# Optimization experiments

Hardware: AMD Instinct MI355X
Metric: run time of the kernel (lower is better)

Reference implementation:

```python
import jax, jax.numpy as jnp
import numpy as np

QMIN, QMAX = -128.0, 127.0  # 8-bit signed activation range


def fq_act(x, s):
    """Fake-quantize activations: clip(round(x/s))*s with straight-through estimator."""
    y = jnp.clip(jnp.round(x / s), QMIN, QMAX) * s
    return x + jax.lax.stop_gradient(y - x)


def fq_weight(w):
    """Per-tensor max-abs symmetric (narrow-range) 8-bit weight fake-quant with STE."""
    s = jnp.max(jnp.abs(w)) / 127.0
    y = jnp.clip(jnp.round(w / s), -127.0, 127.0) * s
    return w + jax.lax.stop_gradient(y - w)


def conv1x1(x, w, b):
    # x: [b,c,h,w], w: [o,c] -> [b,o,h,w]
    return jnp.einsum('bchw,oc->bohw', x, w) + b[None, :, None, None]


def setup_inputs() -> dict:
    key = jax.random.key(0)
    ks = jax.random.split(key, 6)
    B, C, HC, H, W = 8, 64, 32, 64, 64
    x = jax.random.normal(ks[0], (B, C, H, W), dtype=jnp.float32)
    wq = jax.random.normal(ks[1], (HC, C), dtype=jnp.float32) * 0.05
    wk = jax.random.normal(ks[2], (HC, C), dtype=jnp.float32) * 0.05
    wv = jax.random.normal(ks[3], (HC, C), dtype=jnp.float32) * 0.05
    wp = jax.random.normal(ks[4], (C, HC), dtype=jnp.float32) * 0.05
    return {
        'x': x,
        'wq': wq, 'bq': jnp.zeros((HC,), jnp.float32),
        'wk': wk, 'bk': jnp.zeros((HC,), jnp.float32),
        'wv': wv, 'bv': jnp.zeros((HC,), jnp.float32),
        'wp': wp, 'bp': jnp.zeros((C,), jnp.float32),
        's_in': jnp.ones((1,), jnp.float32) * 0.0625,
        's_out': jnp.ones((1,), jnp.float32) * 0.0625,
    }


def reference(x, wq, bq, wk, bk, wv, bv, wp, bp, s_in, s_out):
    b, c, h, w = x.shape
    hc = wq.shape[0]
    n = h * w
    xq = fq_act(x, s_in)                              # quant_inp(x)
    q = conv1x1(xq, fq_weight(wq), bq).reshape(b, hc, n).transpose(0, 2, 1)  # [b,n,hc]
    k = conv1x1(xq, fq_weight(wk), bk).reshape(b, hc, n)                     # [b,hc,n]
    v = conv1x1(xq, fq_weight(wv), bv).reshape(b, hc, n).transpose(0, 2, 1)  # [b,n,hc]
    z = jax.nn.softmax(jnp.einsum('bqc,bck->bqk', q, k), axis=-1)            # [b,n,n]
    z = jnp.einsum('bqk,bkc->bqc', z, v).transpose(0, 2, 1).reshape(b, hc, h, w)
    z = fq_act(z, s_in)                               # quant_inp(z) (shared module/scale)
    out = xq + conv1x1(z, fq_weight(wp), bp)
    return fq_act(out, s_out)                         # self.act QuantIdentity
```

## Files before the change

kernel.cpp:

```cpp
#include <hip/hip_runtime.h>
#include <hip/hip_bf16.h>
#include <cstdint>
#include <cstddef>

#define NB 8
#define NC 64
#define NHC 32
#define NN 4096
#define LOG2E 1.44269504088896340736f

typedef short v8s __attribute__((ext_vector_type(8)));
typedef float v4f __attribute__((ext_vector_type(4)));
typedef unsigned int v4u __attribute__((ext_vector_type(4)));

__device__ __forceinline__ unsigned short f2b(float f) {
    unsigned int u = __builtin_bit_cast(unsigned int, f);
    u += 0x7fffu + ((u >> 16) & 1u);
    return (unsigned short)(u >> 16);
}
__device__ __forceinline__ float b2f(unsigned short s) {
    unsigned int u = ((unsigned int)s) << 16;
    return __builtin_bit_cast(float, u);
}
__device__ __forceinline__ unsigned int pack2_bf16(float a, float b) {
    unsigned int ua = __builtin_bit_cast(unsigned int, a);
    ua += 0x7fffu + ((ua >> 16) & 1u);
    unsigned int ub = __builtin_bit_cast(unsigned int, b);
    ub += 0x7fffu + ((ub >> 16) & 1u);
    return (ua >> 16) | (ub & 0xffff0000u);
}
__device__ __forceinline__ unsigned int trunc2_bf16(float a, float b) {
    return __builtin_amdgcn_perm(__builtin_bit_cast(unsigned int, b),
                                 __builtin_bit_cast(unsigned int, a), 0x07060302u);
}
__device__ __forceinline__ float wave_max(float v) {
    #pragma unroll
    for (int off = 1; off < 64; off <<= 1) v = fmaxf(v, __shfl_xor(v, off));
    return v;
}

__global__ __launch_bounds__(256) void k_qkv(
    const float* __restrict__ x,
    const float* __restrict__ wq, const float* __restrict__ wk, const float* __restrict__ wv,
    const float* __restrict__ bq, const float* __restrict__ bk, const float* __restrict__ bv,
    const float* __restrict__ s_in,
    unsigned short* __restrict__ xqb, unsigned short* __restrict__ qb,
    unsigned short* __restrict__ kb, unsigned short* __restrict__ vb)
{
    int blk = blockIdx.x;
    int b   = blk >> 6;
    int p0  = (blk & 63) * 64;
    int tid = threadIdx.x;
    int wave = tid >> 6;
    int lane = tid & 63;

    __shared__ __align__(16) unsigned short xt[64][72];
    __shared__ __align__(16) unsigned short wlds[6144];
    __shared__ float red[3][4];

    float4 q0 = *(const float4*)(wq + tid * 8), q1 = *(const float4*)(wq + tid * 8 + 4);
    float4 k0 = *(const float4*)(wk + tid * 8), k1 = *(const float4*)(wk + tid * 8 + 4);
    float4 v0 = *(const float4*)(wv + tid * 8), v1 = *(const float4*)(wv + tid * 8 + 4);
    float mq = fmaxf(fmaxf(fmaxf(fabsf(q0.x), fabsf(q0.y)), fmaxf(fabsf(q0.z), fabsf(q0.w))),
                     fmaxf(fmaxf(fabsf(q1.x), fabsf(q1.y)), fmaxf(fabsf(q1.z), fabsf(q1.w))));
    float mk = fmaxf(fmaxf(fmaxf(fabsf(k0.x), fabsf(k0.y)), fmaxf(fabsf(k0.z), fabsf(k0.w))),
                     fmaxf(fmaxf(fabsf(k1.x), fabsf(k1.y)), fmaxf(fabsf(k1.z), fabsf(k1.w))));
    float mv = fmaxf(fmaxf(fmaxf(fabsf(v0.x), fabsf(v0.y)), fmaxf(fabsf(v0.z), fabsf(v0.w))),
                     fmaxf(fmaxf(fabsf(v1.x), fabsf(v1.y)), fmaxf(fabsf(v1.z), fabsf(v1.w))));
    mq = wave_max(mq); mk = wave_max(mk); mv = wave_max(mv);
    if (lane == 0) { red[0][wave] = mq; red[1][wave] = mk; red[2][wave] = mv; }
    __syncthreads();
    float sq = fmaxf(fmaxf(red[0][0], red[0][1]), fmaxf(red[0][2], red[0][3])) / 127.0f;
    float sk = fmaxf(fmaxf(red[1][0], red[1][1]), fmaxf(red[1][2], red[1][3])) / 127.0f;
    float sw = fmaxf(fmaxf(red[2][0], red[2][1]), fmaxf(red[2][2], red[2][3])) / 127.0f;
    {
        float eq[8] = {q0.x, q0.y, q0.z, q0.w, q1.x, q1.y, q1.z, q1.w};
        float ek[8] = {k0.x, k0.y, k0.z, k0.w, k1.x, k1.y, k1.z, k1.w};
        float ev[8] = {v0.x, v0.y, v0.z, v0.w, v1.x, v1.y, v1.z, v1.w};
        #pragma unroll
        for (int j = 0; j < 8; ++j) {
            wlds[0 * 2048 + tid * 8 + j] = f2b(fminf(fmaxf(rintf(eq[j] / sq), -127.f), 127.f) * sq);
            wlds[1 * 2048 + tid * 8 + j] = f2b(fminf(fmaxf(rintf(ek[j] / sk), -127.f), 127.f) * sk);
            wlds[2 * 2048 + tid * 8 + j] = f2b(fminf(fmaxf(rintf(ev[j] / sw), -127.f), 127.f) * sw);
        }
    }

    float sv = s_in[0];
    float sinv = 1.0f / sv;
    int jj = tid & 15;
    int c0 = tid >> 4;
    #pragma unroll
    for (int it = 0; it < 4; ++it) {
        int c = c0 + it * 16;
        size_t gi = ((size_t)(b * NC + c) << 12) + p0 + jj * 4;
        float4 xv = *(const float4*)(x + gi);
        float r0 = fminf(fmaxf(rintf(xv.x * sinv), -128.f), 127.f) * sv;
        float r1 = fminf(fmaxf(rintf(xv.y * sinv), -128.f), 127.f) * sv;
        float r2 = fminf(fmaxf(rintf(xv.z * sinv), -128.f), 127.f) * sv;
        float r3 = fminf(fmaxf(rintf(xv.w * sinv), -128.f), 127.f) * sv;
        *(uint2*)(xqb + gi) = make_uint2(pack2_bf16(r0, r1), pack2_bf16(r2, r3));
        xt[jj * 4 + 0][c] = f2b(r0);
        xt[jj * 4 + 1][c] = f2b(r1);
        xt[jj * 4 + 2][c] = f2b(r2);
        xt[jj * 4 + 3][c] = f2b(r3);
    }
    __syncthreads();

    int quad = lane >> 4;
    int l15  = lane & 15;

    v8s bf0 = *(const v8s*)(&xt[wave * 16 + l15][0  + quad * 8]);
    v8s bf1 = *(const v8s*)(&xt[wave * 16 + l15][32 + quad * 8]);

    int pos = p0 + wave * 16 + l15;
    size_t posg = (size_t)b * NN + pos;
    int posP = p0 + (wave >> 1) * 32 + (l15 >> 2) * 8 + (wave & 1) * 4 + (l15 & 3);
    const v4f zc = {0.f, 0.f, 0.f, 0.f};

    #pragma unroll
    for (int rb = 0; rb < 6; ++rb) {
        v8s a0 = *(const v8s*)(wlds + (rb * 16 + l15) * 64 + 0  + quad * 8);
        v8s a1 = *(const v8s*)(wlds + (rb * 16 + l15) * 64 + 32 + quad * 8);
        v4f t   = __builtin_amdgcn_mfma_f32_16x16x32_bf16(a0, bf0, zc, 0, 0, 0);
        v4f acc = __builtin_amdgcn_mfma_f32_16x16x32_bf16(a1, bf1, t, 0, 0, 0);

        int R0 = rb * 16 + quad * 4;
        float vals[4];
        #pragma unroll
        for (int r = 0; r < 4; ++r) {
            int R = R0 + r;
            float bias = (R < 32) ? bq[R] : (R < 64) ? bk[R - 32] : bv[R - 64];
            float vv = acc[r] + bias;
            if (R < 32) vv *= LOG2E;
            vals[r] = vv;
        }
        if (R0 < 32) {
            *(unsigned int*)(qb + posg * NHC + R0)     = pack2_bf16(vals[0], vals[1]);
            *(unsigned int*)(qb + posg * NHC + R0 + 2) = pack2_bf16(vals[2], vals[3]);
        } else if (R0 < 64) {
            *(unsigned int*)(kb + posg * NHC + R0 - 32)     = pack2_bf16(vals[0], vals[1]);
            *(unsigned int*)(kb + posg * NHC + R0 - 32 + 2) = pack2_bf16(vals[2], vals[3]);
        } else {
            #pragma unroll
            for (int r = 0; r < 4; ++r)
                vb[(size_t)(b * NHC + R0 - 64 + r) * NN + posP] = f2b(vals[r]);
        }
    }
}

__global__ __launch_bounds__(256, 2) void k_attn(
    const unsigned short* __restrict__ qb, const unsigned short* __restrict__ kb,
    const unsigned short* __restrict__ vb, const unsigned short* __restrict__ xqb,
    const float* __restrict__ wp, const float* __restrict__ bp,
    const float* __restrict__ s_in, const float* __restrict__ s_out,
    float* __restrict__ out)
{
    int blk  = blockIdx.x;
    int b    = blk >> 6;
    int qt   = blk & 63;
    int qbase = qt * 64;
    int tid  = threadIdx.x;
    int wave = tid >> 6;
    int lane = tid & 63;
    int quad = lane >> 4;
    int l15  = lane & 15;

    __shared__ __align__(16) float zbuf[4][64][36];
    __shared__ float lbuf[4][64];
    __shared__ __align__(16) unsigned short wpq[2048];
    __shared__ float redw[4];

    {
        float4 a0 = *(const float4*)(wp + tid * 8), a1 = *(const float4*)(wp + tid * 8 + 4);
        float mx = fmaxf(fmaxf(fmaxf(fabsf(a0.x), fabsf(a0.y)), fmaxf(fabsf(a0.z), fabsf(a0.w))),
                         fmaxf(fmaxf(fabsf(a1.x), fabsf(a1.y)), fmaxf(fabsf(a1.z), fabsf(a1.w))));
        mx = wave_max(mx);
        if (lane == 0) redw[wave] = mx;
        __syncthreads();
        float scale = fmaxf(fmaxf(redw[0], redw[1]), fmaxf(redw[2], redw[3])) / 127.0f;
        float e[8] = {a0.x, a0.y, a0.z, a0.w, a1.x, a1.y, a1.z, a1.w};
        #pragma unroll
        for (int j = 0; j < 8; ++j) {
            float r = fminf(fmaxf(rintf(e[j] / scale), -127.f), 127.f);
            wpq[tid * 8 + j] = f2b(r * scale);
        }
    }

    const unsigned short* qbat = qb + (size_t)b * NN * NHC;
    const unsigned short* kbat = kb + (size_t)b * NN * NHC;
    const unsigned short* vbat = vb + (size_t)b * NHC * NN;

    v8s qf[4];
    #pragma unroll
    for (int s = 0; s < 4; ++s)
        qf[s] = *(const v8s*)(qbat + (qbase + s * 16 + l15) * NHC + quad * 8);

    const v4f zc = {0.f, 0.f, 0.f, 0.f};
    v4f zt[4][2] = {{zc, zc}, {zc, zc}, {zc, zc}, {zc, zc}};
    float psA[4] = {0.f, 0.f, 0.f, 0.f};
    float psB[4] = {0.f, 0.f, 0.f, 0.f};

    int k0 = wave * 1024;
    const unsigned short* vrow0 = vbat + (size_t)( 0 + l15) * NN;
    const unsigned short* vrow1 = vbat + (size_t)(16 + l15) * NN;

    v8s ck0 = *(const v8s*)(kbat + (k0 +  0 + l15) * NHC + quad * 8);
    v8s ck1 = *(const v8s*)(kbat + (k0 + 16 + l15) * NHC + quad * 8);
    v8s ck2 = *(const v8s*)(kbat + (k0 + 32 + l15) * NHC + quad * 8);
    v8s ck3 = *(const v8s*)(kbat + (k0 + 48 + l15) * NHC + quad * 8);
    v8s cv00 = *(const v8s*)(vrow0 + k0      + quad * 8);
    v8s cv01 = *(const v8s*)(vrow0 + k0 + 32 + quad * 8);
    v8s cv10 = *(const v8s*)(vrow1 + k0      + quad * 8);
    v8s cv11 = *(const v8s*)(vrow1 + k0 + 32 + quad * 8);

    #pragma unroll 1
    for (int i = 0; i < 16; ++i) {
        int nki = k0 + (((i + 1) & 15) << 6);
        v8s nk0 = *(const v8s*)(kbat + (nki +  0 + l15) * NHC + quad * 8);
        v8s nk1 = *(const v8s*)(kbat + (nki + 16 + l15) * NHC + quad * 8);
        v8s nk2 = *(const v8s*)(kbat + (nki + 32 + l15) * NHC + quad * 8);
        v8s nk3 = *(const v8s*)(kbat + (nki + 48 + l15) * NHC + quad * 8);
        v8s nv00 = *(const v8s*)(vrow0 + nki      + quad * 8);
        v8s nv01 = *(const v8s*)(vrow0 + nki + 32 + quad * 8);
        v8s nv10 = *(const v8s*)(vrow1 + nki      + quad * 8);
        v8s nv11 = *(const v8s*)(vrow1 + nki + 32 + quad * 8);

        #pragma unroll
        for (int s = 0; s < 4; ++s) {
            v4f sa[4];
            __builtin_amdgcn_s_setprio(1);
            sa[0] = __builtin_amdgcn_mfma_f32_16x16x32_bf16(ck0, qf[s], zc, 0, 0, 0);
            sa[1] = __builtin_amdgcn_mfma_f32_16x16x32_bf16(ck1, qf[s], zc, 0, 0, 0);
            sa[2] = __builtin_amdgcn_mfma_f32_16x16x32_bf16(ck2, qf[s], zc, 0, 0, 0);
            sa[3] = __builtin_amdgcn_mfma_f32_16x16x32_bf16(ck3, qf[s], zc, 0, 0, 0);
            __builtin_amdgcn_s_setprio(0);

            #pragma unroll
            for (int g = 0; g < 2; ++g) {
                float p00 = __builtin_amdgcn_exp2f(sa[2 * g][0]);
                float p01 = __builtin_amdgcn_exp2f(sa[2 * g][1]);
                float p02 = __builtin_amdgcn_exp2f(sa[2 * g][2]);
                float p03 = __builtin_amdgcn_exp2f(sa[2 * g][3]);
                float p10 = __builtin_amdgcn_exp2f(sa[2 * g + 1][0]);
                float p11 = __builtin_amdgcn_exp2f(sa[2 * g + 1][1]);
                float p12 = __builtin_amdgcn_exp2f(sa[2 * g + 1][2]);
                float p13 = __builtin_amdgcn_exp2f(sa[2 * g + 1][3]);
                psA[s] += p00 + p01;
                psB[s] += p02 + p03;
                psA[s] += p10 + p11;
                psB[s] += p12 + p13;
                v4u w;
                w.x = trunc2_bf16(p00, p01);
                w.y = trunc2_bf16(p02, p03);
                w.z = trunc2_bf16(p10, p11);
                w.w = trunc2_bf16(p12, p13);
                v8s pfrag = __builtin_bit_cast(v8s, w);
                __builtin_amdgcn_s_setprio(1);
                if (g == 0) {
                    zt[s][0] = __builtin_amdgcn_mfma_f32_16x16x32_bf16(cv00, pfrag, zt[s][0], 0, 0, 0);
                    zt[s][1] = __builtin_amdgcn_mfma_f32_16x16x32_bf16(cv10, pfrag, zt[s][1], 0, 0, 0);
                } else {
                    zt[s][0] = __builtin_amdgcn_mfma_f32_16x16x32_bf16(cv01, pfrag, zt[s][0], 0, 0, 0);
                    zt[s][1] = __builtin_amdgcn_mfma_f32_16x16x32_bf16(cv11, pfrag, zt[s][1], 0, 0, 0);
                }
                __builtin_amdgcn_s_setprio(0);
            }
        }
        ck0 = nk0; ck1 = nk1; ck2 = nk2; ck3 = nk3;
        cv00 = nv00; cv01 = nv01; cv10 = nv10; cv11 = nv11;
    }

    #pragma unroll
    for (int s = 0; s < 4; ++s) {
        *(v4f*)(&zbuf[wave][s * 16 + l15][     quad * 4]) = zt[s][0];
        *(v4f*)(&zbuf[wave][s * 16 + l15][16 + quad * 4]) = zt[s][1];
        float ps = psA[s] + psB[s];
        ps += __shfl_xor(ps, 16);
        ps += __shfl_xor(ps, 32);
        if (quad == 0) lbuf[wave][s * 16 + l15] = ps;
    }
    __syncthreads();

    int myq = wave * 16 + l15;
    float L = lbuf[0][myq] + lbuf[1][myq] + lbuf[2][myq] + lbuf[3][myq];

    float z[8] = {0.f};
    #pragma unroll
    for (int w = 0; w < 4; ++w) {
        v4f za  = *(const v4f*)(&zbuf[w][myq][quad * 8]);
        v4f zb2 = *(const v4f*)(&zbuf[w][myq][quad * 8 + 4]);
        #pragma unroll
        for (int j = 0; j < 4; ++j) { z[j] += za[j]; z[4 + j] += zb2[j]; }
    }
    float sv = s_in[0], sinv = 1.0f / sv;
    float so = s_out[0], soinv = 1.0f / so;
    float Linv = 1.0f / L;
    unsigned int zp[4];
    #pragma unroll
    for (int jp = 0; jp < 4; ++jp) {
        float a = z[2 * jp]     * Linv;
        float c = z[2 * jp + 1] * Linv;
        a = fminf(fmaxf(rintf(a * sinv), -128.f), 127.f) * sv;
        c = fminf(fmaxf(rintf(c * sinv), -128.f), 127.f) * sv;
        zp[jp] = pack2_bf16(a, c);
    }
    v8s zf = __builtin_bit_cast(v8s, *(uint4*)zp);

    v8s w0f = *(const v8s*)(wpq + ( 0 + l15) * NHC + quad * 8);
    v8s w1f = *(const v8s*)(wpq + (16 + l15) * NHC + quad * 8);
    v8s w2f = *(const v8s*)(wpq + (32 + l15) * NHC + quad * 8);
    v8s w3f = *(const v8s*)(wpq + (48 + l15) * NHC + quad * 8);
    v4f o0 = __builtin_amdgcn_mfma_f32_16x16x32_bf16(w0f, zf, zc, 0, 0, 0);
    v4f o1 = __builtin_amdgcn_mfma_f32_16x16x32_bf16(w1f, zf, zc, 0, 0, 0);
    v4f o2 = __builtin_amdgcn_mfma_f32_16x16x32_bf16(w2f, zf, zc, 0, 0, 0);
    v4f o3 = __builtin_amdgcn_mfma_f32_16x16x32_bf16(w3f, zf, zc, 0, 0, 0);

    int pos = qbase + wave * 16 + l15;
    #pragma unroll
    for (int ot = 0; ot < 4; ++ot) {
        v4f ov = (ot == 0) ? o0 : (ot == 1) ? o1 : (ot == 2) ? o2 : o3;
        #pragma unroll
        for (int r = 0; r < 4; ++r) {
            int oc = ot * 16 + quad * 4 + r;
            size_t idx = (size_t)(b * NC + oc) * NN + pos;
            float val = ov[r] + bp[oc] + b2f(xqb[idx]);
            float f = fminf(fmaxf(rintf(val * soinv), -128.f), 127.f);
            out[idx] = f * so;
        }
    }
}

extern "C" void kernel_launch(void* const* d_in, const int* in_sizes, int n_in,
                              void* d_out, int out_size, void* d_ws, size_t ws_size,
                              hipStream_t stream) {
    const float* x     = (const float*)d_in[0];
    const float* wq    = (const float*)d_in[1];
    const float* bq    = (const float*)d_in[2];
    const float* wk    = (const float*)d_in[3];
    const float* bk    = (const float*)d_in[4];
    const float* wv    = (const float*)d_in[5];
    const float* bv    = (const float*)d_in[6];
    const float* wp    = (const float*)d_in[7];
    const float* bp    = (const float*)d_in[8];
    const float* s_in  = (const float*)d_in[9];
    const float* s_out = (const float*)d_in[10];
    float* out = (float*)d_out;

    char* ws = (char*)d_ws;
    size_t off = 0;
    auto carve = [&](size_t bytes) {
        void* p = ws + off;
        off = (off + bytes + 255) & ~(size_t)255;
        return p;
    };
    unsigned short* xqb = (unsigned short*)carve((size_t)NB * NC * NN * 2);
    unsigned short* qbf = (unsigned short*)carve((size_t)NB * NN * NHC * 2);
    unsigned short* kbf = (unsigned short*)carve((size_t)NB * NN * NHC * 2);
    unsigned short* vbf = (unsigned short*)carve((size_t)NB * NHC * NN * 2);

    hipLaunchKernelGGL(k_qkv, dim3(512), dim3(256), 0, stream,
                       x, wq, wk, wv, bq, bk, bv, s_in, xqb, qbf, kbf, vbf);
    hipLaunchKernelGGL(k_attn, dim3(512), dim3(256), 0, stream,
                       qbf, kbf, vbf, xqb, wp, bp, s_in, s_out, out);
}
```

Measured before the change: 112.4 us.

## Halve QKV projection tile to 32 positions and interleave batch in block index

```diff
diff --git a/kernel.cpp b/kernel.cpp
--- a/kernel.cpp
+++ b/kernel.cpp
@@ -39,7 +39,7 @@
     return v;
 }
 
-__global__ __launch_bounds__(256) void k_qkv(
+__global__ __launch_bounds__(256, 4) void k_qkv(
     const float* __restrict__ x,
     const float* __restrict__ wq, const float* __restrict__ wk, const float* __restrict__ wv,
     const float* __restrict__ bq, const float* __restrict__ bk, const float* __restrict__ bv,
@@ -48,19 +48,26 @@
     unsigned short* __restrict__ kb, unsigned short* __restrict__ vb)
 {
     int blk = blockIdx.x;
-    int b   = blk >> 6;
-    int p0  = (blk & 63) * 64;
+    int b   = blk & 7;
+    int p0  = (blk >> 3) * 32;
     int tid = threadIdx.x;
     int wave = tid >> 6;
     int lane = tid & 63;
 
-    __shared__ __align__(16) unsigned short xt[64][72];
+    __shared__ __align__(16) unsigned short xt[32][72];
     __shared__ __align__(16) unsigned short wlds[6144];
     __shared__ float red[3][4];
 
     float4 q0 = *(const float4*)(wq + tid * 8), q1 = *(const float4*)(wq + tid * 8 + 4);
     float4 k0 = *(const float4*)(wk + tid * 8), k1 = *(const float4*)(wk + tid * 8 + 4);
     float4 v0 = *(const float4*)(wv + tid * 8), v1 = *(const float4*)(wv + tid * 8 + 4);
+    int jj = tid & 7;
+    int c0 = tid >> 3;
+    size_t gi0 = ((size_t)(b * NC + c0) << 12) + p0 + jj * 4;
+    size_t gi1 = ((size_t)(b * NC + c0 + 32) << 12) + p0 + jj * 4;
+    float4 xv0 = *(const float4*)(x + gi0);
+    float4 xv1 = *(const float4*)(x + gi1);
+
     float mq = fmaxf(fmaxf(fmaxf(fabsf(q0.x), fabsf(q0.y)), fmaxf(fabsf(q0.z), fabsf(q0.w))),
                      fmaxf(fmaxf(fabsf(q1.x), fabsf(q1.y)), fmaxf(fabsf(q1.z), fabsf(q1.w))));
     float mk = fmaxf(fmaxf(fmaxf(fabsf(k0.x), fabsf(k0.y)), fmaxf(fabsf(k0.z), fabsf(k0.w))),
@@ -87,38 +94,46 @@
 
     float sv = s_in[0];
     float sinv = 1.0f / sv;
-    int jj = tid & 15;
-    int c0 = tid >> 4;
-    #pragma unroll
-    for (int it = 0; it < 4; ++it) {
-        int c = c0 + it * 16;
-        size_t gi = ((size_t)(b * NC + c) << 12) + p0 + jj * 4;
-        float4 xv = *(const float4*)(x + gi);
-        float r0 = fminf(fmaxf(rintf(xv.x * sinv), -128.f), 127.f) * sv;
-        float r1 = fminf(fmaxf(rintf(xv.y * sinv), -128.f), 127.f) * sv;
-        float r2 = fminf(fmaxf(rintf(xv.z * sinv), -128.f), 127.f) * sv;
-        float r3 = fminf(fmaxf(rintf(xv.w * sinv), -128.f), 127.f) * sv;
-        *(uint2*)(xqb + gi) = make_uint2(pack2_bf16(r0, r1), pack2_bf16(r2, r3));
-        xt[jj * 4 + 0][c] = f2b(r0);
-        xt[jj * 4 + 1][c] = f2b(r1);
-        xt[jj * 4 + 2][c] = f2b(r2);
-        xt[jj * 4 + 3][c] = f2b(r3);
+    {
+        float r0 = fminf(fmaxf(rintf(xv0.x * sinv), -128.f), 127.f) * sv;
+        float r1 = fminf(fmaxf(rintf(xv0.y * sinv), -128.f), 127.f) * sv;
+        float r2 = fminf(fmaxf(rintf(xv0.z * sinv), -128.f), 127.f) * sv;
+        float r3 = fminf(fmaxf(rintf(xv0.w * sinv), -128.f), 127.f) * sv;
+        *(uint2*)(xqb + gi0) = make_uint2(pack2_bf16(r0, r1), pack2_bf16(r2, r3));
+        xt[jj * 4 + 0][c0] = f2b(r0);
+        xt[jj * 4 + 1][c0] = f2b(r1);
+        xt[jj * 4 + 2][c0] = f2b(r2);
+        xt[jj * 4 + 3][c0] = f2b(r3);
+        float u0 = fminf(fmaxf(rintf(xv1.x * sinv), -128.f), 127.f) * sv;
+        float u1 = fminf(fmaxf(rintf(xv1.y * sinv), -128.f), 127.f) * sv;
+        float u2 = fminf(fmaxf(rintf(xv1.z * sinv), -128.f), 127.f) * sv;
+        float u3 = fminf(fmaxf(rintf(xv1.w * sinv), -128.f), 127.f) * sv;
+        *(uint2*)(xqb + gi1) = make_uint2(pack2_bf16(u0, u1), pack2_bf16(u2, u3));
+        xt[jj * 4 + 0][c0 + 32] = f2b(u0);
+        xt[jj * 4 + 1][c0 + 32] = f2b(u1);
+        xt[jj * 4 + 2][c0 + 32] = f2b(u2);
+        xt[jj * 4 + 3][c0 + 32] = f2b(u3);
     }
     __syncthreads();
 
     int quad = lane >> 4;
     int l15  = lane & 15;
-
-    v8s bf0 = *(const v8s*)(&xt[wave * 16 + l15][0  + quad * 8]);
-    v8s bf1 = *(const v8s*)(&xt[wave * 16 + l15][32 + quad * 8]);
-
-    int pos = p0 + wave * 16 + l15;
+    int ps   = wave >> 1;
+    int rh   = wave & 1;
+
+    v8s bf0 = *(const v8s*)(&xt[ps * 16 + l15][0  + quad * 8]);
+    v8s bf1 = *(const v8s*)(&xt[ps * 16 + l15][32 + quad * 8]);
+
+    int pos = p0 + ps * 16 + l15;
     size_t posg = (size_t)b * NN + pos;
-    int posP = p0 + (wave >> 1) * 32 + (l15 >> 2) * 8 + (wave & 1) * 4 + (l15 & 3);
+    int T   = p0 & ~63;
+    int tau = ((p0 & 32) >> 4) + ps;
+    int posP = T + (tau >> 1) * 32 + (l15 >> 2) * 8 + (tau & 1) * 4 + (l15 & 3);
     const v4f zc = {0.f, 0.f, 0.f, 0.f};
 
     #pragma unroll
-    for (int rb = 0; rb < 6; ++rb) {
+    for (int j = 0; j < 3; ++j) {
+        int rb = rh * 3 + j;
         v8s a0 = *(const v8s*)(wlds + (rb * 16 + l15) * 64 + 0  + quad * 8);
         v8s a1 = *(const v8s*)(wlds + (rb * 16 + l15) * 64 + 32 + quad * 8);
         v4f t   = __builtin_amdgcn_mfma_f32_16x16x32_bf16(a0, bf0, zc, 0, 0, 0);
@@ -156,8 +171,8 @@
     float* __restrict__ out)
 {
     int blk  = blockIdx.x;
-    int b    = blk >> 6;
-    int qt   = blk & 63;
+    int b    = blk & 7;
+    int qt   = blk >> 3;
     int qbase = qt * 64;
     int tid  = threadIdx.x;
     int wave = tid >> 6;
@@ -358,7 +373,7 @@
     unsigned short* kbf = (unsigned short*)carve((size_t)NB * NN * NHC * 2);
     unsigned short* vbf = (unsigned short*)carve((size_t)NB * NHC * NN * 2);
 
-    hipLaunchKernelGGL(k_qkv, dim3(512), dim3(256), 0, stream,
+    hipLaunchKernelGGL(k_qkv, dim3(1024), dim3(256), 0, stream,
                        x, wq, wk, wv, bq, bk, bv, s_in, xqb, qbf, kbf, vbf);
     hipLaunchKernelGGL(k_attn, dim3(512), dim3(256), 0, stream,
                        qbf, kbf, vbf, xqb, wp, bp, s_in, s_out, out);
```

After: 117.0 us. 1.04x slower.

## Store K and V in MFMA-fragment-packed layout and interleave batches across blocks

Applied to the files above, without the earlier changes.

```diff
diff --git a/kernel.cpp b/kernel.cpp
--- a/kernel.cpp
+++ b/kernel.cpp
@@ -48,8 +48,9 @@
     unsigned short* __restrict__ kb, unsigned short* __restrict__ vb)
 {
     int blk = blockIdx.x;
-    int b   = blk >> 6;
-    int p0  = (blk & 63) * 64;
+    int b   = blk & 7;
+    int seg = blk >> 3;
+    int p0  = seg * 64;
     int tid = threadIdx.x;
     int wave = tid >> 6;
     int lane = tid & 63;
@@ -114,7 +115,12 @@
 
     int pos = p0 + wave * 16 + l15;
     size_t posg = (size_t)b * NN + pos;
-    int posP = p0 + (wave >> 1) * 32 + (l15 >> 2) * 8 + (wave & 1) * 4 + (l15 & 3);
+    int g_v  = wave >> 1;
+    int hi_v = wave & 1;
+    int qs   = l15 >> 2;
+    int rr   = l15 & 3;
+    int jv   = hi_v * 4 + rr;
+    size_t fb = (size_t)b * NN * NHC + (size_t)seg * 2048;
     const v4f zc = {0.f, 0.f, 0.f, 0.f};
 
     #pragma unroll
@@ -138,12 +144,18 @@
             *(unsigned int*)(qb + posg * NHC + R0)     = pack2_bf16(vals[0], vals[1]);
             *(unsigned int*)(qb + posg * NHC + R0 + 2) = pack2_bf16(vals[2], vals[3]);
         } else if (R0 < 64) {
-            *(unsigned int*)(kb + posg * NHC + R0 - 32)     = pack2_bf16(vals[0], vals[1]);
-            *(unsigned int*)(kb + posg * NHC + R0 - 32 + 2) = pack2_bf16(vals[2], vals[3]);
+            int chb = R0 - 32;
+            size_t sidx = fb + (size_t)wave * 512 + ((chb >> 3) * 16 + l15) * 8 + (chb & 7);
+            *(uint2*)(kb + sidx) = make_uint2(pack2_bf16(vals[0], vals[1]),
+                                              pack2_bf16(vals[2], vals[3]));
         } else {
+            int h = rb - 4;
             #pragma unroll
-            for (int r = 0; r < 4; ++r)
-                vb[(size_t)(b * NHC + R0 - 64 + r) * NN + posP] = f2b(vals[r]);
+            for (int r = 0; r < 4; ++r) {
+                int lp = quad * 4 + r;
+                size_t sidx = fb + (size_t)(2 * h + g_v) * 512 + (qs * 16 + lp) * 8 + jv;
+                vb[sidx] = f2b(vals[r]);
+            }
         }
     }
 }
@@ -156,8 +168,8 @@
     float* __restrict__ out)
 {
     int blk  = blockIdx.x;
-    int b    = blk >> 6;
-    int qt   = blk & 63;
+    int b    = blk & 7;
+    int qt   = blk >> 3;
     int qbase = qt * 64;
     int tid  = threadIdx.x;
     int wave = tid >> 6;
@@ -187,8 +199,8 @@
     }
 
     const unsigned short* qbat = qb + (size_t)b * NN * NHC;
-    const unsigned short* kbat = kb + (size_t)b * NN * NHC;
-    const unsigned short* vbat = vb + (size_t)b * NHC * NN;
+    const unsigned short* kft  = kb + (size_t)b * NN * NHC;
+    const unsigned short* vft  = vb + (size_t)b * NN * NHC;
 
     v8s qf[4];
     #pragma unroll
@@ -200,30 +212,33 @@
     float psA[4] = {0.f, 0.f, 0.f, 0.f};
     float psB[4] = {0.f, 0.f, 0.f, 0.f};
 
-    int k0 = wave * 1024;
-    const unsigned short* vrow0 = vbat + (size_t)( 0 + l15) * NN;
-    const unsigned short* vrow1 = vbat + (size_t)(16 + l15) * NN;
-
-    v8s ck0 = *(const v8s*)(kbat + (k0 +  0 + l15) * NHC + quad * 8);
-    v8s ck1 = *(const v8s*)(kbat + (k0 + 16 + l15) * NHC + quad * 8);
-    v8s ck2 = *(const v8s*)(kbat + (k0 + 32 + l15) * NHC + quad * 8);
-    v8s ck3 = *(const v8s*)(kbat + (k0 + 48 + l15) * NHC + quad * 8);
-    v8s cv00 = *(const v8s*)(vrow0 + k0      + quad * 8);
-    v8s cv01 = *(const v8s*)(vrow0 + k0 + 32 + quad * 8);
-    v8s cv10 = *(const v8s*)(vrow1 + k0      + quad * 8);
-    v8s cv11 = *(const v8s*)(vrow1 + k0 + 32 + quad * 8);
+    int lane8 = lane * 8;
+    int t0 = wave * 16;
+
+    const unsigned short* kp = kft + (size_t)t0 * 2048;
+    const unsigned short* vp = vft + (size_t)t0 * 2048;
+    v8s ck0 = *(const v8s*)(kp + 0 * 512 + lane8);
+    v8s ck1 = *(const v8s*)(kp + 1 * 512 + lane8);
+    v8s ck2 = *(const v8s*)(kp + 2 * 512 + lane8);
+    v8s ck3 = *(const v8s*)(kp + 3 * 512 + lane8);
+    v8s cv00 = *(const v8s*)(vp + 0 * 512 + lane8);
+    v8s cv01 = *(const v8s*)(vp + 1 * 512 + lane8);
+    v8s cv10 = *(const v8s*)(vp + 2 * 512 + lane8);
+    v8s cv11 = *(const v8s*)(vp + 3 * 512 + lane8);
 
     #pragma unroll 1
     for (int i = 0; i < 16; ++i) {
-        int nki = k0 + (((i + 1) & 15) << 6);
-        v8s nk0 = *(const v8s*)(kbat + (nki +  0 + l15) * NHC + quad * 8);
-        v8s nk1 = *(const v8s*)(kbat + (nki + 16 + l15) * NHC + quad * 8);
-        v8s nk2 = *(const v8s*)(kbat + (nki + 32 + l15) * NHC + quad * 8);
-        v8s nk3 = *(const v8s*)(kbat + (nki + 48 + l15) * NHC + quad * 8);
-        v8s nv00 = *(const v8s*)(vrow0 + nki      + quad * 8);
-        v8s nv01 = *(const v8s*)(vrow0 + nki + 32 + quad * 8);
-        v8s nv10 = *(const v8s*)(vrow1 + nki      + quad * 8);
-        v8s nv11 = *(const v8s*)(vrow1 + nki + 32 + quad * 8);
+        int ni = wave * 16 + ((i + 1) & 15);
+        const unsigned short* kn = kft + (size_t)ni * 2048;
+        const unsigned short* vn = vft + (size_t)ni * 2048;
+        v8s nk0 = *(const v8s*)(kn + 0 * 512 + lane8);
+        v8s nk1 = *(const v8s*)(kn + 1 * 512 + lane8);
+        v8s nk2 = *(const v8s*)(kn + 2 * 512 + lane8);
+        v8s nk3 = *(const v8s*)(kn + 3 * 512 + lane8);
+        v8s nv00 = *(const v8s*)(vn + 0 * 512 + lane8);
+        v8s nv01 = *(const v8s*)(vn + 1 * 512 + lane8);
+        v8s nv10 = *(const v8s*)(vn + 2 * 512 + lane8);
+        v8s nv11 = *(const v8s*)(vn + 3 * 512 + lane8);
 
         #pragma unroll
         for (int s = 0; s < 4; ++s) {
```

After: 113.4 us. About the same (+0.9%).
